# Optimization experiments

Measured on AMD Instinct MI355X. Metric: run time of the kernel, lower is better.

The kernel has to match this reference:

```python
import jax, jax.numpy as jnp
import numpy as np

N = 50000   # n_nodes
E = 500000  # n_edges
D = 128     # input_dim == hidden_dim
L = 2       # n_layers
K = 5       # Chebyshev filter size


def setup_inputs() -> dict:
    key = jax.random.key(0)
    k0, k1, k2, k3, k4 = jax.random.split(key, 5)
    scale = 1.0 / np.sqrt(D)
    return {
        "edge_index": jax.random.randint(k0, (2, E), 0, N),
        "edge_weight": jax.random.uniform(k1, (E,), dtype=jnp.float32),
        "emb": jax.random.uniform(k2, (N, D), dtype=jnp.float32, minval=-1.0, maxval=1.0),
        "Wx": jax.random.normal(k3, (L, 3, K, D, D), dtype=jnp.float32) * scale,
        "bx": jnp.zeros((L, 3, D), dtype=jnp.float32),
        "Wh": jax.random.normal(k4, (L, 3, K, D, D), dtype=jnp.float32) * scale,
        "bh": jnp.zeros((L, 3, D), dtype=jnp.float32),
    }


def reference(edge_index, edge_weight, emb, Wx, bx, Wh, bh):
    src, dst = edge_index[0], edge_index[1]
    # ChebConv sym-normalized scaled Laplacian with lambda_max=2:
    # L_hat = L - I = -D^{-1/2} A D^{-1/2} (zero diagonal)
    deg = jax.ops.segment_sum(edge_weight, src, num_segments=N)
    dinv = jnp.where(deg > 0, deg ** -0.5, 0.0)
    w = -dinv[src] * edge_weight * dinv[dst]  # [E]

    def prop(x):  # L_hat @ x via gather/scatter over edges
        return jax.ops.segment_sum(w[:, None] * x[src], dst, num_segments=N)

    def cheb(x, W, b):  # sum_k T_k(L_hat) x W_k + b
        Tx0 = x
        out = Tx0 @ W[0]
        Tx1 = prop(Tx0)
        out = out + Tx1 @ W[1]
        for k in range(2, K):
            Tx2 = 2.0 * prop(Tx1) - Tx0
            out = out + Tx2 @ W[k]
            Tx0, Tx1 = Tx1, Tx2
        return out + b

    x = emb
    hidden_states = []
    for l in range(L):
        H = jnp.ones((N, D), x.dtype)  # init__hidd: ones
        Z = jax.nn.sigmoid(cheb(x, Wx[l, 0], bx[l, 0]) + cheb(H, Wh[l, 0], bh[l, 0]))
        R = jax.nn.sigmoid(cheb(x, Wx[l, 1], bx[l, 1]) + cheb(H, Wh[l, 1], bh[l, 1]))
        Ht = jnp.tanh(cheb(x, Wx[l, 2], bx[l, 2]) + cheb(H * R, Wh[l, 2], bh[l, 2]))
        Hn = Z * H + (1.0 - Z) * Ht
        h = jax.nn.relu(Hn)  # dropout is identity in eval mode
        hidden_states.append(h)
        x = h
    return x  # == hidden_states[-1]
```

## Files before the change

### kernel.cpp

```cpp
#include <hip/hip_runtime.h>
#include <math.h>

#define NN 50000
#define EE 500000
#define DD 128
#define KK 5
#define LL 2

typedef _Float16 f16x8 __attribute__((ext_vector_type(8)));
typedef float f32x4 __attribute__((ext_vector_type(4)));

__device__ __forceinline__ ushort f2h(float x) {
    union { _Float16 h; ushort u; } v; v.h = (_Float16)x; return v.u;
}


__global__ __launch_bounds__(256) void edge_pass1(
    const int* __restrict__ src, const int* __restrict__ dst,
    const float* __restrict__ ew,
    float* __restrict__ deg, int* __restrict__ hist)
{
    int e = blockIdx.x * blockDim.x + threadIdx.x;
    if (e >= EE) return;
    atomicAdd(&deg[src[e]], ew[e]);
    atomicAdd(&hist[dst[e]], 1);
}

__global__ __launch_bounds__(256) void dinv_kernel(
    const float* __restrict__ deg, float* __restrict__ dinv)
{
    int i = blockIdx.x * blockDim.x + threadIdx.x;
    if (i >= NN) return;
    float d = deg[i];
    dinv[i] = (d > 0.f) ? (1.f / sqrtf(d)) : 0.f;
}

#define SCAN_C ((NN + 1023) / 1024)
__global__ __launch_bounds__(1024) void scan_kernel(
    const int* __restrict__ hist, int* __restrict__ row_ptr)
{
    __shared__ int sums[1024];
    const int t = threadIdx.x;
    const int base = t * SCAN_C;
    int local[SCAN_C];
    int s = 0;
#pragma unroll
    for (int j = 0; j < SCAN_C; ++j) {
        int i = base + j;
        int v = (i < NN) ? hist[i] : 0;
        s += v;
        local[j] = s;
    }
    sums[t] = s;
    __syncthreads();
    for (int off = 1; off < 1024; off <<= 1) {
        int v = (t >= off) ? sums[t - off] : 0;
        __syncthreads();
        sums[t] += v;
        __syncthreads();
    }
    int excl = sums[t] - s;
    if (t == 0) row_ptr[0] = 0;
#pragma unroll
    for (int j = 0; j < SCAN_C; ++j) {
        int i = base + j;
        if (i < NN) row_ptr[i + 1] = excl + local[j];
    }
}

__global__ __launch_bounds__(256) void copy_fill(
    const int* __restrict__ row_ptr, int* __restrict__ fill)
{
    int i = blockIdx.x * blockDim.x + threadIdx.x;
    if (i < NN) fill[i] = row_ptr[i];
}

__global__ __launch_bounds__(256) void edge_scatter(
    const int* __restrict__ src, const int* __restrict__ dst,
    const float* __restrict__ ew, const float* __restrict__ dinv,
    int* __restrict__ fill,
    int* __restrict__ src_srt, float* __restrict__ w_srt)
{
    int e = blockIdx.x * blockDim.x + threadIdx.x;
    if (e >= EE) return;
    int s = src[e], t = dst[e];
    float w = -dinv[s] * ew[e] * dinv[t];
    int pos = atomicAdd(&fill[t], 1);
    src_srt[pos] = s;
    w_srt[pos] = w;
}

__global__ __launch_bounds__(256) void propv_kernel(
    const int* __restrict__ rp, const int* __restrict__ ss, const float* __restrict__ sw,
    const float* __restrict__ tin, const float* __restrict__ tprev, float* __restrict__ tout,
    float alpha, float beta, int ones_in, int ones_prev)
{
    int i = blockIdx.x * blockDim.x + threadIdx.x;
    if (i >= NN) return;
    float acc = 0.f;
    int e0 = rp[i], e1 = rp[i + 1];
    int e = e0;
    for (; e + 4 <= e1; e += 4) {
        float t0 = ones_in ? 1.f : tin[ss[e]];
        float t1v = ones_in ? 1.f : tin[ss[e + 1]];
        float t2v = ones_in ? 1.f : tin[ss[e + 2]];
        float t3v = ones_in ? 1.f : tin[ss[e + 3]];
        acc += sw[e] * t0 + sw[e + 1] * t1v + sw[e + 2] * t2v + sw[e + 3] * t3v;
    }
    for (; e < e1; ++e) {
        float tv = ones_in ? 1.f : tin[ss[e]];
        acc += sw[e] * tv;
    }
    float pv = ones_prev ? 1.f : (tprev ? tprev[i] : 0.f);
    tout[i] = alpha * acc + beta * pv;
}

__global__ __launch_bounds__(128) void colsum_kernel(
    const float* __restrict__ Wh, float* __restrict__ scol)
{
    int b = blockIdx.x;
    int k = b % KK;
    int g = (b / KK) % 2;
    int l = b / (2 * KK);
    int d = threadIdx.x;
    const float* Wp = Wh + ((size_t)((l * 3 + g) * KK + k)) * DD * DD;
    float s = 0.f;
    for (int r = 0; r < DD; ++r) s += Wp[r * DD + d];
    scol[((size_t)((l * 2 + g) * KK + k)) * DD + d] = s;
}

__global__ __launch_bounds__(256) void wconv_f16(
    const float* __restrict__ W, ushort* __restrict__ out, int mode)
{
    int t = blockIdx.x;
    int st = (mode == 0) ? t : ((t / KK) * 3 + 2) * KK + (t % KK);
    const float* Wp = W + (size_t)st * DD * DD;
    ushort* op = out + (size_t)t * DD * DD;
    for (int idx = threadIdx.x; idx < DD * DD; idx += 256) {
        int rb = idx >> 7, c = idx & 127;
        float w = Wp[c * DD + rb];
        int byte = rb * 256 + (((c * 2) ^ ((rb & 7) << 4)));
        *(ushort*)((char*)op + byte) = f2h(w);
    }
}

__global__ __launch_bounds__(256) void f32_to_f16(
    const float* __restrict__ in, ushort* __restrict__ out, int n8)
{
    int i = blockIdx.x * blockDim.x + threadIdx.x;
    if (i >= n8) return;
    float4 a = ((const float4*)in)[i * 2];
    float4 b = ((const float4*)in)[i * 2 + 1];
    f16x8 o;
    o[0] = (_Float16)a.x; o[1] = (_Float16)a.y; o[2] = (_Float16)a.z; o[3] = (_Float16)a.w;
    o[4] = (_Float16)b.x; o[5] = (_Float16)b.y; o[6] = (_Float16)b.z; o[7] = (_Float16)b.w;
    ((f16x8*)out)[i] = o;
}

__global__ __launch_bounds__(256) void prop_mat(
    const int* __restrict__ rp, const int* __restrict__ ss, const float* __restrict__ sw,
    const ushort* __restrict__ x, const ushort* __restrict__ prev,
    ushort* __restrict__ out, float alpha, float beta)
{
    int node = blockIdx.x * 16 + (threadIdx.x >> 4);
    if (node >= NN) return;
    int lane = threadIdx.x & 15;
    int c = lane * 8;
    float acc[8];
#pragma unroll
    for (int j = 0; j < 8; ++j) acc[j] = 0.f;
    int e0 = rp[node], e1 = rp[node + 1];
    int e = e0;
    for (; e + 8 <= e1; e += 8) {
        int s0 = ss[e], s1 = ss[e + 1], s2 = ss[e + 2], s3 = ss[e + 3];
        int s4 = ss[e + 4], s5 = ss[e + 5], s6 = ss[e + 6], s7 = ss[e + 7];
        float w0 = sw[e], w1 = sw[e + 1], w2 = sw[e + 2], w3 = sw[e + 3];
        float w4 = sw[e + 4], w5 = sw[e + 5], w6 = sw[e + 6], w7 = sw[e + 7];
        f16x8 r0 = *(const f16x8*)(x + (size_t)s0 * DD + c);
        f16x8 r1 = *(const f16x8*)(x + (size_t)s1 * DD + c);
        f16x8 r2 = *(const f16x8*)(x + (size_t)s2 * DD + c);
        f16x8 r3 = *(const f16x8*)(x + (size_t)s3 * DD + c);
        f16x8 r4 = *(const f16x8*)(x + (size_t)s4 * DD + c);
        f16x8 r5 = *(const f16x8*)(x + (size_t)s5 * DD + c);
        f16x8 r6 = *(const f16x8*)(x + (size_t)s6 * DD + c);
        f16x8 r7 = *(const f16x8*)(x + (size_t)s7 * DD + c);
#pragma unroll
        for (int j = 0; j < 8; ++j)
            acc[j] += w0 * (float)r0[j] + w1 * (float)r1[j] + w2 * (float)r2[j] + w3 * (float)r3[j]
                    + w4 * (float)r4[j] + w5 * (float)r5[j] + w6 * (float)r6[j] + w7 * (float)r7[j];
    }
    for (; e + 4 <= e1; e += 4) {
        int s0 = ss[e], s1 = ss[e + 1], s2 = ss[e + 2], s3 = ss[e + 3];
        float w0 = sw[e], w1 = sw[e + 1], w2 = sw[e + 2], w3 = sw[e + 3];
        f16x8 r0 = *(const f16x8*)(x + (size_t)s0 * DD + c);
        f16x8 r1 = *(const f16x8*)(x + (size_t)s1 * DD + c);
        f16x8 r2 = *(const f16x8*)(x + (size_t)s2 * DD + c);
        f16x8 r3 = *(const f16x8*)(x + (size_t)s3 * DD + c);
#pragma unroll
        for (int j = 0; j < 8; ++j)
            acc[j] += w0 * (float)r0[j] + w1 * (float)r1[j] + w2 * (float)r2[j] + w3 * (float)r3[j];
    }
    for (; e < e1; ++e) {
        int s = ss[e];
        float w = sw[e];
        f16x8 r = *(const f16x8*)(x + (size_t)s * DD + c);
#pragma unroll
        for (int j = 0; j < 8; ++j) acc[j] += w * (float)r[j];
    }
    f16x8 o;
    if (beta != 0.f && prev) {
        f16x8 pv = *(const f16x8*)(prev + (size_t)node * DD + c);
#pragma unroll
        for (int j = 0; j < 8; ++j) o[j] = (_Float16)(alpha * acc[j] + beta * (float)pv[j]);
    } else {
#pragma unroll
        for (int j = 0; j < 8; ++j) o[j] = (_Float16)(alpha * acc[j]);
    }
    *(f16x8*)(out + (size_t)node * DD + c) = o;
}

__device__ __forceinline__ void mm_gate(
    const ushort* __restrict__ const* Ts, const ushort* __restrict__ Wg,
    ushort* Bs, int rowg0, int rowg1, bool ok0, bool ok1,
    int tid, int lk, f32x4 acc[2][8], int lr)
{
#pragma unroll
    for (int fr = 0; fr < 2; ++fr)
#pragma unroll
        for (int fc = 0; fc < 8; ++fc) acc[fr][fc] = (f32x4){0.f, 0.f, 0.f, 0.f};
#pragma unroll
    for (int k = 0; k < KK; ++k) {
        const ushort* Bg = Wg + (size_t)k * (DD * DD);
        __syncthreads();
#pragma unroll
        for (int i = 0; i < 8; ++i) {
            int off = i * 4096 + tid * 16;
            uint4 v = *(const uint4*)((const char*)Bg + off);
            *(uint4*)((char*)Bs + off) = v;
        }
        f16x8 a[2][4];
#pragma unroll
        for (int fr = 0; fr < 2; ++fr) {
            int rowg = fr ? rowg1 : rowg0;
            bool ok = fr ? ok1 : ok0;
            const ushort* rp2 = Ts[k] + (size_t)rowg * DD + lk * 8;
#pragma unroll
            for (int ko = 0; ko < 4; ++ko) {
                if (ok) a[fr][ko] = *(const f16x8*)(rp2 + ko * 32);
                else a[fr][ko] = (f16x8){0, 0, 0, 0, 0, 0, 0, 0};
            }
        }
        __syncthreads();
#pragma unroll
        for (int ko = 0; ko < 4; ++ko) {
            const int cb = ko * 64 + lk * 16;
#pragma unroll
            for (int fc = 0; fc < 8; ++fc) {
                int rb = fc * 16 + lr;
                int byte = (rb * 256 + cb) ^ ((rb & 7) << 4);
                f16x8 bfrag = *(const f16x8*)((const char*)Bs + byte);
                acc[0][fc] = __builtin_amdgcn_mfma_f32_16x16x32_f16(a[0][ko], bfrag, acc[0][fc], 0, 0, 0);
                acc[1][fc] = __builtin_amdgcn_mfma_f32_16x16x32_f16(a[1][ko], bfrag, acc[1][fc], 0, 0, 0);
            }
        }
    }
}

__device__ __forceinline__ int xcd_swz(int b, int nwg) {
    int xcd = b & 7, idx = b >> 3;
    int q = nwg >> 3, rr = nwg & 7;
    int start = (xcd < rr) ? xcd * (q + 1) : rr * (q + 1) + (xcd - rr) * q;
    return start + idx;
}

__global__ __launch_bounds__(256) void cheb_mm_mfma(
    const ushort* __restrict__ T0, const ushort* __restrict__ T1,
    const ushort* __restrict__ T2, const ushort* __restrict__ T3,
    const ushort* __restrict__ T4,
    const ushort* __restrict__ Wt, int gate_stride,
    float* __restrict__ outbase, size_t out_stride, int ngates)
{
    __shared__ ushort Bs[DD * DD];
    const int lin = xcd_swz(blockIdx.x, gridDim.x);
    const int tile = lin / ngates;
    const int g = lin - tile * ngates;

    const int tid = threadIdx.x;
    const int lane = tid & 63;
    const int wid = tid >> 6;
    const int lr = lane & 15;
    const int lk = lane >> 4;
    const int r0 = tile * 128;
    const ushort* Ts[5] = {T0, T1, T2, T3, T4};

    int rowg0 = r0 + wid * 32 + lr;
    int rowg1 = rowg0 + 16;
    bool ok0 = rowg0 < NN;
    bool ok1 = rowg1 < NN;

    f32x4 acc[2][8];
    mm_gate(Ts, Wt + (size_t)g * gate_stride, Bs, rowg0, rowg1, ok0, ok1, tid, lk, acc, lr);

    float* outp = outbase + (size_t)g * out_stride;
#pragma unroll
    for (int fr = 0; fr < 2; ++fr) {
#pragma unroll
        for (int j = 0; j < 4; ++j) {
            int grow = r0 + wid * 32 + fr * 16 + lk * 4 + j;
            if (grow < NN) {
#pragma unroll
                for (int fc = 0; fc < 8; ++fc) {
                    int col = fc * 16 + lr;
                    outp[(size_t)grow * DD + col] = acc[fr][fc][j];
                }
            }
        }
    }
}

__global__ __launch_bounds__(256) void cheb_mm_final(
    const ushort* __restrict__ T0, const ushort* __restrict__ T1,
    const ushort* __restrict__ T2, const ushort* __restrict__ T3,
    const ushort* __restrict__ T4,
    const ushort* __restrict__ Wt,
    const float* __restrict__ Xh, const float* __restrict__ Xz,
    const float* __restrict__ bx, const float* __restrict__ bh, int l,
    float* __restrict__ out, ushort* __restrict__ h16, int write_f32)
{
    __shared__ ushort Bs[DD * DD];
    const int tile = xcd_swz(blockIdx.x, gridDim.x);
    const int tid = threadIdx.x;
    const int lane = tid & 63;
    const int wid = tid >> 6;
    const int lr = lane & 15;
    const int lk = lane >> 4;
    const int r0 = tile * 128;
    const ushort* Ts[5] = {T0, T1, T2, T3, T4};

    int rowg0 = r0 + wid * 32 + lr;
    int rowg1 = rowg0 + 16;
    bool ok0 = rowg0 < NN;
    bool ok1 = rowg1 < NN;

    f32x4 acc[2][8];
    mm_gate(Ts, Wt, Bs, rowg0, rowg1, ok0, ok1, tid, lk, acc, lr);

    const float* b0 = bx + (size_t)(l * 3 + 2) * DD;
    const float* b1 = bh + (size_t)(l * 3 + 2) * DD;
#pragma unroll
    for (int fr = 0; fr < 2; ++fr) {
#pragma unroll
        for (int j = 0; j < 4; ++j) {
            int grow = r0 + wid * 32 + fr * 16 + lk * 4 + j;
            if (grow < NN) {
#pragma unroll
                for (int fc = 0; fc < 8; ++fc) {
                    int d = fc * 16 + lr;
                    size_t idx = (size_t)grow * DD + d;
                    float pre = acc[fr][fc][j] + Xh[idx] + b0[d] + b1[d];
                    float ht = tanhf(pre);
                    float z = Xz[idx];
                    float hn = z + (1.f - z) * ht;
                    float h = hn > 0.f ? hn : 0.f;
                    if (write_f32) out[idx] = h;
                    h16[idx] = f2h(h);
                }
            }
        }
    }
}

__global__ __launch_bounds__(256) void gate_zr_kernel(
    float* __restrict__ Xz, const float* __restrict__ Xr, ushort* __restrict__ Xr_f16,
    const float* __restrict__ tvec, const float* __restrict__ scol,
    const float* __restrict__ bx, const float* __restrict__ bh, int l)
{
    int idx = blockIdx.x * blockDim.x + threadIdx.x;
    if (idx >= NN * DD) return;
    int i = idx >> 7;
    int d = idx & 127;
    float t1 = tvec[i], t2 = tvec[NN + i], t3 = tvec[2 * NN + i], t4 = tvec[3 * NN + i];

    const float* s0 = scol + (size_t)((l * 2 + 0) * KK) * DD;
    float hz = s0[d] + t1 * s0[DD + d] + t2 * s0[2 * DD + d] + t3 * s0[3 * DD + d] + t4 * s0[4 * DD + d];
    float z = Xz[idx] + bx[(l * 3 + 0) * DD + d] + bh[(l * 3 + 0) * DD + d] + hz;
    Xz[idx] = 1.f / (1.f + expf(-z));

    const float* s1 = scol + (size_t)((l * 2 + 1) * KK) * DD;
    float hr = s1[d] + t1 * s1[DD + d] + t2 * s1[2 * DD + d] + t3 * s1[3 * DD + d] + t4 * s1[4 * DD + d];
    float r = Xr[idx] + bx[(l * 3 + 1) * DD + d] + bh[(l * 3 + 1) * DD + d] + hr;
    Xr_f16[idx] = f2h(1.f / (1.f + expf(-r)));
}


extern "C" void kernel_launch(void* const* d_in, const int* in_sizes, int n_in,
                              void* d_out, int out_size, void* d_ws, size_t ws_size,
                              hipStream_t stream)
{
    const int*   ei  = (const int*)d_in[0];
    const float* ew  = (const float*)d_in[1];
    const float* emb = (const float*)d_in[2];
    const float* Wx  = (const float*)d_in[3];
    const float* bx  = (const float*)d_in[4];
    const float* Wh  = (const float*)d_in[5];
    const float* bh  = (const float*)d_in[6];
    float* out = (float*)d_out;

    const int* src = ei;
    const int* dst = ei + EE;

    char* ws = (char*)d_ws;
    size_t off = 0;
    auto alloc = [&](size_t nbytes) -> char* {
        char* p = ws + off;
        off = (off + nbytes + 255) & ~(size_t)255;
        return p;
    };
    float*  deg     = (float*)alloc((size_t)NN * 4);
    float*  dinv    = (float*)alloc((size_t)NN * 4);
    int*    hist    = (int*)alloc((size_t)(NN + 1) * 4);
    int*    row_ptr = (int*)alloc((size_t)(NN + 1) * 4);
    int*    fill    = (int*)alloc((size_t)(NN + 1) * 4);
    int*    src_srt = (int*)alloc((size_t)EE * 4);
    float*  w_srt   = (float*)alloc((size_t)EE * 4);
    float*  tvec    = (float*)alloc((size_t)4 * NN * 4);
    float*  scol    = (float*)alloc((size_t)LL * 2 * KK * DD * 4);
    float*  X       = (float*)alloc((size_t)3 * NN * DD * 4);
    ushort* Th      = (ushort*)alloc((size_t)4 * NN * DD * 2);
    ushort* x_f16   = (ushort*)alloc((size_t)NN * DD * 2);
    ushort* Xr_f16  = (ushort*)alloc((size_t)NN * DD * 2);
    ushort* WxT     = (ushort*)alloc((size_t)LL * 3 * KK * DD * DD * 2);
    ushort* WhT2    = (ushort*)alloc((size_t)LL * KK * DD * DD * 2);
    (void)ws_size; (void)in_sizes; (void)n_in; (void)out_size;

    float* Xz = X;
    float* Xr = X + (size_t)NN * DD;
    float* Xh = X + (size_t)2 * NN * DD;
    ushort* T1 = Th;
    ushort* T2 = Th + (size_t)NN * DD;
    ushort* T3 = Th + (size_t)2 * NN * DD;
    ushort* T4 = Th + (size_t)3 * NN * DD;

    const int EG = (EE + 255) / 256;
    const int NG = (NN + 255) / 256;
    const int PG = (NN + 15) / 16;
    const int ELG = (NN * DD + 255) / 256;
    const int MMG = (NN + 127) / 128;
    const int CVG = (NN * DD / 8 + 255) / 256;
    const int GATE_STRIDE = KK * DD * DD;

    hipMemsetAsync(deg, 0, (size_t)NN * 4, stream);
    hipMemsetAsync(hist, 0, (size_t)(NN + 1) * 4, stream);

    edge_pass1<<<EG, 256, 0, stream>>>(src, dst, ew, deg, hist);
    dinv_kernel<<<NG, 256, 0, stream>>>(deg, dinv);
    scan_kernel<<<1, 1024, 0, stream>>>(hist, row_ptr);
    copy_fill<<<NG, 256, 0, stream>>>(row_ptr, fill);
    edge_scatter<<<EG, 256, 0, stream>>>(src, dst, ew, dinv, fill, src_srt, w_srt);

    float* t1 = tvec;
    float* t2 = tvec + NN;
    float* t3 = tvec + 2 * NN;
    float* t4 = tvec + 3 * NN;
    propv_kernel<<<NG, 256, 0, stream>>>(row_ptr, src_srt, w_srt, nullptr, nullptr, t1, 1.f,  0.f, 1, 0);
    propv_kernel<<<NG, 256, 0, stream>>>(row_ptr, src_srt, w_srt, t1, nullptr,      t2, 2.f, -1.f, 0, 1);
    propv_kernel<<<NG, 256, 0, stream>>>(row_ptr, src_srt, w_srt, t2, t1,           t3, 2.f, -1.f, 0, 0);
    propv_kernel<<<NG, 256, 0, stream>>>(row_ptr, src_srt, w_srt, t3, t2,           t4, 2.f, -1.f, 0, 0);

    colsum_kernel<<<LL * 2 * KK, 128, 0, stream>>>(Wh, scol);

    wconv_f16<<<LL * 3 * KK, 256, 0, stream>>>(Wx, WxT, 0);
    wconv_f16<<<LL * KK, 256, 0, stream>>>(Wh, WhT2, 1);

    f32_to_f16<<<CVG, 256, 0, stream>>>(emb, x_f16, NN * DD / 8);

    for (int l = 0; l < LL; ++l) {
        prop_mat<<<PG, 256, 0, stream>>>(row_ptr, src_srt, w_srt, x_f16, nullptr, T1, 1.f,  0.f);
        prop_mat<<<PG, 256, 0, stream>>>(row_ptr, src_srt, w_srt, T1,    x_f16,   T2, 2.f, -1.f);
        prop_mat<<<PG, 256, 0, stream>>>(row_ptr, src_srt, w_srt, T2,    T1,      T3, 2.f, -1.f);
        prop_mat<<<PG, 256, 0, stream>>>(row_ptr, src_srt, w_srt, T3,    T2,      T4, 2.f, -1.f);

        cheb_mm_mfma<<<MMG * 3, 256, 0, stream>>>(x_f16, T1, T2, T3, T4,
                                             WxT + (size_t)l * 3 * GATE_STRIDE, GATE_STRIDE,
                                             Xz, (size_t)NN * DD, 3);

        gate_zr_kernel<<<ELG, 256, 0, stream>>>(Xz, Xr, Xr_f16, tvec, scol, bx, bh, l);

        prop_mat<<<PG, 256, 0, stream>>>(row_ptr, src_srt, w_srt, Xr_f16, nullptr, T1, 1.f,  0.f);
        prop_mat<<<PG, 256, 0, stream>>>(row_ptr, src_srt, w_srt, T1,     Xr_f16,  T2, 2.f, -1.f);
        prop_mat<<<PG, 256, 0, stream>>>(row_ptr, src_srt, w_srt, T2,     T1,      T3, 2.f, -1.f);
        prop_mat<<<PG, 256, 0, stream>>>(row_ptr, src_srt, w_srt, T3,     T2,      T4, 2.f, -1.f);

        cheb_mm_final<<<MMG, 256, 0, stream>>>(Xr_f16, T1, T2, T3, T4,
                                               WhT2 + (size_t)l * GATE_STRIDE,
                                               Xh, Xz, bx, bh, l,
                                               out, x_f16, (l == LL - 1) ? 1 : 0);
    }
}
```

Before: 863.9 us.

## Store f16 node features in 16-column panels to localize SpMM gathers

The f16 feature matrices (x, T1..T4, Xr) now use a panel layout: 8 panels of 16 columns, each stored contiguously over all nodes. prop_mat gives each block one panel and 128 nodes, with two threads per node, so the gathered working set per panel is a 1.6 MB slice that can stay in cache instead of scattering across full 256-byte rows. The MFMA and gate kernels are adapted to read and write this layout. cheb_mm_final now uses 64-row tiles so more blocks are launched. Each gathered access is now only 32 bytes, and the edge index and weight lists are re-read once for each of the 8 panels.

After: 927.4 us. 1.07x slower.

```diff
diff --git a/kernel.cpp b/kernel.cpp
--- a/kernel.cpp
+++ b/kernel.cpp
@@ -6,6 +6,8 @@
 #define DD 128
 #define KK 5
 #define LL 2
+
+#define PSZ ((size_t)NN * 16)
 
 typedef _Float16 f16x8 __attribute__((ext_vector_type(8)));
 typedef float f32x4 __attribute__((ext_vector_type(4)));
@@ -144,17 +146,20 @@
     }
 }
 
-__global__ __launch_bounds__(256) void f32_to_f16(
+__global__ __launch_bounds__(256) void f32_to_f16_panel(
     const float* __restrict__ in, ushort* __restrict__ out, int n8)
 {
-    int i = blockIdx.x * blockDim.x + threadIdx.x;
-    if (i >= n8) return;
-    float4 a = ((const float4*)in)[i * 2];
-    float4 b = ((const float4*)in)[i * 2 + 1];
+    int j = blockIdx.x * blockDim.x + threadIdx.x;
+    if (j >= n8) return;
+    int flat = j * 8;
+    int i = flat >> 7;
+    int d0 = flat & 127;
+    float4 a = *(const float4*)(in + (size_t)i * DD + d0);
+    float4 b = *(const float4*)(in + (size_t)i * DD + d0 + 4);
     f16x8 o;
     o[0] = (_Float16)a.x; o[1] = (_Float16)a.y; o[2] = (_Float16)a.z; o[3] = (_Float16)a.w;
     o[4] = (_Float16)b.x; o[5] = (_Float16)b.y; o[6] = (_Float16)b.z; o[7] = (_Float16)b.w;
-    ((f16x8*)out)[i] = o;
+    *(f16x8*)(out + (size_t)(d0 >> 4) * PSZ + (size_t)i * 16 + (d0 & 15)) = o;
 }
 
 __global__ __launch_bounds__(256) void prop_mat(
@@ -162,10 +167,11 @@
     const ushort* __restrict__ x, const ushort* __restrict__ prev,
     ushort* __restrict__ out, float alpha, float beta)
 {
-    int node = blockIdx.x * 16 + (threadIdx.x >> 4);
+    const int p = blockIdx.x & 7;
+    const int node = (blockIdx.x >> 3) * 128 + (threadIdx.x >> 1);
     if (node >= NN) return;
-    int lane = threadIdx.x & 15;
-    int c = lane * 8;
+    const int half = (threadIdx.x & 1) * 8;
+    const ushort* xp = x + (size_t)p * PSZ + half;
     float acc[8];
 #pragma unroll
     for (int j = 0; j < 8; ++j) acc[j] = 0.f;
@@ -176,14 +182,14 @@
         int s4 = ss[e + 4], s5 = ss[e + 5], s6 = ss[e + 6], s7 = ss[e + 7];
         float w0 = sw[e], w1 = sw[e + 1], w2 = sw[e + 2], w3 = sw[e + 3];
         float w4 = sw[e + 4], w5 = sw[e + 5], w6 = sw[e + 6], w7 = sw[e + 7];
-        f16x8 r0 = *(const f16x8*)(x + (size_t)s0 * DD + c);
-        f16x8 r1 = *(const f16x8*)(x + (size_t)s1 * DD + c);
-        f16x8 r2 = *(const f16x8*)(x + (size_t)s2 * DD + c);
-        f16x8 r3 = *(const f16x8*)(x + (size_t)s3 * DD + c);
-        f16x8 r4 = *(const f16x8*)(x + (size_t)s4 * DD + c);
-        f16x8 r5 = *(const f16x8*)(x + (size_t)s5 * DD + c);
-        f16x8 r6 = *(const f16x8*)(x + (size_t)s6 * DD + c);
-        f16x8 r7 = *(const f16x8*)(x + (size_t)s7 * DD + c);
+        f16x8 r0 = *(const f16x8*)(xp + (size_t)s0 * 16);
+        f16x8 r1 = *(const f16x8*)(xp + (size_t)s1 * 16);
+        f16x8 r2 = *(const f16x8*)(xp + (size_t)s2 * 16);
+        f16x8 r3 = *(const f16x8*)(xp + (size_t)s3 * 16);
+        f16x8 r4 = *(const f16x8*)(xp + (size_t)s4 * 16);
+        f16x8 r5 = *(const f16x8*)(xp + (size_t)s5 * 16);
+        f16x8 r6 = *(const f16x8*)(xp + (size_t)s6 * 16);
+        f16x8 r7 = *(const f16x8*)(xp + (size_t)s7 * 16);
 #pragma unroll
         for (int j = 0; j < 8; ++j)
             acc[j] += w0 * (float)r0[j] + w1 * (float)r1[j] + w2 * (float)r2[j] + w3 * (float)r3[j]
@@ -192,10 +198,10 @@
     for (; e + 4 <= e1; e += 4) {
         int s0 = ss[e], s1 = ss[e + 1], s2 = ss[e + 2], s3 = ss[e + 3];
         float w0 = sw[e], w1 = sw[e + 1], w2 = sw[e + 2], w3 = sw[e + 3];
-        f16x8 r0 = *(const f16x8*)(x + (size_t)s0 * DD + c);
-        f16x8 r1 = *(const f16x8*)(x + (size_t)s1 * DD + c);
-        f16x8 r2 = *(const f16x8*)(x + (size_t)s2 * DD + c);
-        f16x8 r3 = *(const f16x8*)(x + (size_t)s3 * DD + c);
+        f16x8 r0 = *(const f16x8*)(xp + (size_t)s0 * 16);
+        f16x8 r1 = *(const f16x8*)(xp + (size_t)s1 * 16);
+        f16x8 r2 = *(const f16x8*)(xp + (size_t)s2 * 16);
+        f16x8 r3 = *(const f16x8*)(xp + (size_t)s3 * 16);
 #pragma unroll
         for (int j = 0; j < 8; ++j)
             acc[j] += w0 * (float)r0[j] + w1 * (float)r1[j] + w2 * (float)r2[j] + w3 * (float)r3[j];
@@ -203,29 +209,30 @@
     for (; e < e1; ++e) {
         int s = ss[e];
         float w = sw[e];
-        f16x8 r = *(const f16x8*)(x + (size_t)s * DD + c);
+        f16x8 r = *(const f16x8*)(xp + (size_t)s * 16);
 #pragma unroll
         for (int j = 0; j < 8; ++j) acc[j] += w * (float)r[j];
     }
     f16x8 o;
     if (beta != 0.f && prev) {
-        f16x8 pv = *(const f16x8*)(prev + (size_t)node * DD + c);
+        f16x8 pv = *(const f16x8*)(prev + (size_t)p * PSZ + (size_t)node * 16 + half);
 #pragma unroll
         for (int j = 0; j < 8; ++j) o[j] = (_Float16)(alpha * acc[j] + beta * (float)pv[j]);
     } else {
 #pragma unroll
         for (int j = 0; j < 8; ++j) o[j] = (_Float16)(alpha * acc[j]);
     }
-    *(f16x8*)(out + (size_t)node * DD + c) = o;
-}
-
+    *(f16x8*)(out + (size_t)p * PSZ + (size_t)node * 16 + half) = o;
+}
+
+template<int NFR>
 __device__ __forceinline__ void mm_gate(
     const ushort* __restrict__ const* Ts, const ushort* __restrict__ Wg,
-    ushort* Bs, int rowg0, int rowg1, bool ok0, bool ok1,
-    int tid, int lk, f32x4 acc[2][8], int lr)
-{
-#pragma unroll
-    for (int fr = 0; fr < 2; ++fr)
+    ushort* Bs, const int* rowg, const bool* ok,
+    int tid, int lk, f32x4 acc[NFR][8], int lr)
+{
+#pragma unroll
+    for (int fr = 0; fr < NFR; ++fr)
 #pragma unroll
         for (int fc = 0; fc < 8; ++fc) acc[fr][fc] = (f32x4){0.f, 0.f, 0.f, 0.f};
 #pragma unroll
@@ -238,15 +245,15 @@
             uint4 v = *(const uint4*)((const char*)Bg + off);
             *(uint4*)((char*)Bs + off) = v;
         }
-        f16x8 a[2][4];
-#pragma unroll
-        for (int fr = 0; fr < 2; ++fr) {
-            int rowg = fr ? rowg1 : rowg0;
-            bool ok = fr ? ok1 : ok0;
-            const ushort* rp2 = Ts[k] + (size_t)rowg * DD + lk * 8;
+        f16x8 a[NFR][4];
+#pragma unroll
+        for (int fr = 0; fr < NFR; ++fr) {
 #pragma unroll
             for (int ko = 0; ko < 4; ++ko) {
-                if (ok) a[fr][ko] = *(const f16x8*)(rp2 + ko * 32);
+                int col0 = lk * 8 + ko * 32;
+                const ushort* ap = Ts[k] + (size_t)(col0 >> 4) * PSZ
+                                 + (size_t)rowg[fr] * 16 + (col0 & 15);
+                if (ok[fr]) a[fr][ko] = *(const f16x8*)ap;
                 else a[fr][ko] = (f16x8){0, 0, 0, 0, 0, 0, 0, 0};
             }
         }
@@ -259,8 +266,9 @@
                 int rb = fc * 16 + lr;
                 int byte = (rb * 256 + cb) ^ ((rb & 7) << 4);
                 f16x8 bfrag = *(const f16x8*)((const char*)Bs + byte);
-                acc[0][fc] = __builtin_amdgcn_mfma_f32_16x16x32_f16(a[0][ko], bfrag, acc[0][fc], 0, 0, 0);
-                acc[1][fc] = __builtin_amdgcn_mfma_f32_16x16x32_f16(a[1][ko], bfrag, acc[1][fc], 0, 0, 0);
+#pragma unroll
+                for (int fr = 0; fr < NFR; ++fr)
+                    acc[fr][fc] = __builtin_amdgcn_mfma_f32_16x16x32_f16(a[fr][ko], bfrag, acc[fr][fc], 0, 0, 0);
             }
         }
     }
@@ -293,13 +301,11 @@
     const int r0 = tile * 128;
     const ushort* Ts[5] = {T0, T1, T2, T3, T4};
 
-    int rowg0 = r0 + wid * 32 + lr;
-    int rowg1 = rowg0 + 16;
-    bool ok0 = rowg0 < NN;
-    bool ok1 = rowg1 < NN;
+    int rowg[2] = {r0 + wid * 32 + lr, r0 + wid * 32 + lr + 16};
+    bool ok[2] = {rowg[0] < NN, rowg[1] < NN};
 
     f32x4 acc[2][8];
-    mm_gate(Ts, Wt + (size_t)g * gate_stride, Bs, rowg0, rowg1, ok0, ok1, tid, lk, acc, lr);
+    mm_gate<2>(Ts, Wt + (size_t)g * gate_stride, Bs, rowg, ok, tid, lk, acc, lr);
 
     float* outp = outbase + (size_t)g * out_stride;
 #pragma unroll
@@ -334,37 +340,32 @@
     const int wid = tid >> 6;
     const int lr = lane & 15;
     const int lk = lane >> 4;
-    const int r0 = tile * 128;
+    const int r0 = tile * 64;
     const ushort* Ts[5] = {T0, T1, T2, T3, T4};
 
-    int rowg0 = r0 + wid * 32 + lr;
-    int rowg1 = rowg0 + 16;
-    bool ok0 = rowg0 < NN;
-    bool ok1 = rowg1 < NN;
-
-    f32x4 acc[2][8];
-    mm_gate(Ts, Wt, Bs, rowg0, rowg1, ok0, ok1, tid, lk, acc, lr);
+    int rowg[1] = {r0 + wid * 16 + lr};
+    bool ok[1] = {rowg[0] < NN};
+
+    f32x4 acc[1][8];
+    mm_gate<1>(Ts, Wt, Bs, rowg, ok, tid, lk, acc, lr);
 
     const float* b0 = bx + (size_t)(l * 3 + 2) * DD;
     const float* b1 = bh + (size_t)(l * 3 + 2) * DD;
 #pragma unroll
-    for (int fr = 0; fr < 2; ++fr) {
-#pragma unroll
-        for (int j = 0; j < 4; ++j) {
-            int grow = r0 + wid * 32 + fr * 16 + lk * 4 + j;
-            if (grow < NN) {
-#pragma unroll
-                for (int fc = 0; fc < 8; ++fc) {
-                    int d = fc * 16 + lr;
-                    size_t idx = (size_t)grow * DD + d;
-                    float pre = acc[fr][fc][j] + Xh[idx] + b0[d] + b1[d];
-                    float ht = tanhf(pre);
-                    float z = Xz[idx];
-                    float hn = z + (1.f - z) * ht;
-                    float h = hn > 0.f ? hn : 0.f;
-                    if (write_f32) out[idx] = h;
-                    h16[idx] = f2h(h);
-                }
+    for (int j = 0; j < 4; ++j) {
+        int grow = r0 + wid * 16 + lk * 4 + j;
+        if (grow < NN) {
+#pragma unroll
+            for (int fc = 0; fc < 8; ++fc) {
+                int d = fc * 16 + lr;
+                size_t idx = (size_t)grow * DD + d;
+                float pre = acc[0][fc][j] + Xh[idx] + b0[d] + b1[d];
+                float ht = tanhf(pre);
+                float z = Xz[idx];
+                float hn = z + (1.f - z) * ht;
+                float h = hn > 0.f ? hn : 0.f;
+                if (write_f32) out[idx] = h;
+                else h16[(size_t)fc * PSZ + (size_t)grow * 16 + lr] = f2h(h);
             }
         }
     }
@@ -389,7 +390,7 @@
     const float* s1 = scol + (size_t)((l * 2 + 1) * KK) * DD;
     float hr = s1[d] + t1 * s1[DD + d] + t2 * s1[2 * DD + d] + t3 * s1[3 * DD + d] + t4 * s1[4 * DD + d];
     float r = Xr[idx] + bx[(l * 3 + 1) * DD + d] + bh[(l * 3 + 1) * DD + d] + hr;
-    Xr_f16[idx] = f2h(1.f / (1.f + expf(-r)));
+    Xr_f16[(size_t)(d >> 4) * PSZ + (size_t)i * 16 + (d & 15)] = f2h(1.f / (1.f + expf(-r)));
 }
 
 
@@ -443,9 +444,10 @@
 
     const int EG = (EE + 255) / 256;
     const int NG = (NN + 255) / 256;
-    const int PG = (NN + 15) / 16;
+    const int PG = ((NN + 127) / 128) * 8;
     const int ELG = (NN * DD + 255) / 256;
     const int MMG = (NN + 127) / 128;
+    const int MMG2 = (NN + 63) / 64;
     const int CVG = (NN * DD / 8 + 255) / 256;
     const int GATE_STRIDE = KK * DD * DD;
 
@@ -472,7 +474,7 @@
     wconv_f16<<<LL * 3 * KK, 256, 0, stream>>>(Wx, WxT, 0);
     wconv_f16<<<LL * KK, 256, 0, stream>>>(Wh, WhT2, 1);
 
-    f32_to_f16<<<CVG, 256, 0, stream>>>(emb, x_f16, NN * DD / 8);
+    f32_to_f16_panel<<<CVG, 256, 0, stream>>>(emb, x_f16, NN * DD / 8);
 
     for (int l = 0; l < LL; ++l) {
         prop_mat<<<PG, 256, 0, stream>>>(row_ptr, src_srt, w_srt, x_f16, nullptr, T1, 1.f,  0.f);
@@ -491,7 +493,7 @@
         prop_mat<<<PG, 256, 0, stream>>>(row_ptr, src_srt, w_srt, T2,     T1,      T3, 2.f, -1.f);
         prop_mat<<<PG, 256, 0, stream>>>(row_ptr, src_srt, w_srt, T3,     T2,      T4, 2.f, -1.f);
 
-        cheb_mm_final<<<MMG, 256, 0, stream>>>(Xr_f16, T1, T2, T3, T4,
+        cheb_mm_final<<<MMG2, 256, 0, stream>>>(Xr_f16, T1, T2, T3, T4,
                                                WhT2 + (size_t)l * GATE_STRIDE,
                                                Xh, Xz, bx, bh, l,
                                                out, x_f16, (l == LL - 1) ? 1 : 0);
```

## Degree-bucket prop rows, pre-fragment weights, drop LDS staging in cheb matmuls

Applied to the files above, without the earlier changes.

Nodes are sorted into degree buckets through a histogram, scan and scatter, and prop_mat walks them in that order so that the 16-lane groups in a block have similar edge counts. Weights are now stored in MFMA fragment order, which lets the matmul kernels read B fragments straight from global memory (through cache) with no LDS staging or __syncthreads. cheb_mm_final moves to 64-row tiles with one fragment row per wave, doubling its grid. The final layer no longer writes the unused f16 copy. The costs are scattered node order in prop_mat writes, repeated global loads of weights per wave, and three extra setup kernels.

Result: slower. 1.312 ms (+51.8%).

```diff
diff --git a/kernel.cpp b/kernel.cpp
--- a/kernel.cpp
+++ b/kernel.cpp
@@ -88,6 +88,44 @@
     int pos = atomicAdd(&fill[t], 1);
     src_srt[pos] = s;
     w_srt[pos] = w;
+}
+
+__global__ __launch_bounds__(256) void deg_bucket(
+    const int* __restrict__ row_ptr, int* __restrict__ bhist)
+{
+    int i = blockIdx.x * blockDim.x + threadIdx.x;
+    if (i >= NN) return;
+    int d = row_ptr[i + 1] - row_ptr[i];
+    if (d > 255) d = 255;
+    atomicAdd(&bhist[d], 1);
+}
+
+__global__ __launch_bounds__(256) void bucket_scan(
+    const int* __restrict__ bhist, int* __restrict__ bfill)
+{
+    __shared__ int buf[256];
+    int t = threadIdx.x;
+    int v0 = bhist[t];
+    buf[t] = v0;
+    __syncthreads();
+    for (int off = 1; off < 256; off <<= 1) {
+        int v = (t >= off) ? buf[t - off] : 0;
+        __syncthreads();
+        buf[t] += v;
+        __syncthreads();
+    }
+    bfill[t] = buf[t] - v0;
+}
+
+__global__ __launch_bounds__(256) void bucket_scatter(
+    const int* __restrict__ row_ptr, int* __restrict__ bfill, int* __restrict__ perm)
+{
+    int i = blockIdx.x * blockDim.x + threadIdx.x;
+    if (i >= NN) return;
+    int d = row_ptr[i + 1] - row_ptr[i];
+    if (d > 255) d = 255;
+    int pos = atomicAdd(&bfill[d], 1);
+    perm[pos] = i;
 }
 
 __global__ __launch_bounds__(256) void propv_kernel(
@@ -129,7 +167,7 @@
     scol[((size_t)((l * 2 + g) * KK + k)) * DD + d] = s;
 }
 
-__global__ __launch_bounds__(256) void wconv_f16(
+__global__ __launch_bounds__(256) void wconv_frag(
     const float* __restrict__ W, ushort* __restrict__ out, int mode)
 {
     int t = blockIdx.x;
@@ -137,10 +175,14 @@
     const float* Wp = W + (size_t)st * DD * DD;
     ushort* op = out + (size_t)t * DD * DD;
     for (int idx = threadIdx.x; idx < DD * DD; idx += 256) {
-        int rb = idx >> 7, c = idx & 127;
-        float w = Wp[c * DD + rb];
-        int byte = rb * 256 + (((c * 2) ^ ((rb & 7) << 4)));
-        *(ushort*)((char*)op + byte) = f2h(w);
+        int j  = idx & 7;
+        int lk = (idx >> 3) & 3;
+        int lr = (idx >> 5) & 15;
+        int fc = (idx >> 9) & 7;
+        int ko = idx >> 12;
+        int dout = fc * 16 + lr;
+        int din  = ko * 32 + lk * 8 + j;
+        op[idx] = f2h(Wp[din * DD + dout]);
     }
 }
 
@@ -159,11 +201,13 @@
 
 __global__ __launch_bounds__(256) void prop_mat(
     const int* __restrict__ rp, const int* __restrict__ ss, const float* __restrict__ sw,
+    const int* __restrict__ perm,
     const ushort* __restrict__ x, const ushort* __restrict__ prev,
     ushort* __restrict__ out, float alpha, float beta)
 {
-    int node = blockIdx.x * 16 + (threadIdx.x >> 4);
-    if (node >= NN) return;
+    int dense = blockIdx.x * 16 + (threadIdx.x >> 4);
+    if (dense >= NN) return;
+    int node = perm[dense];
     int lane = threadIdx.x & 15;
     int c = lane * 8;
     float acc[8];
@@ -219,48 +263,37 @@
     *(f16x8*)(out + (size_t)node * DD + c) = o;
 }
 
+template<int NFR>
 __device__ __forceinline__ void mm_gate(
     const ushort* __restrict__ const* Ts, const ushort* __restrict__ Wg,
-    ushort* Bs, int rowg0, int rowg1, bool ok0, bool ok1,
-    int tid, int lk, f32x4 acc[2][8], int lr)
-{
-#pragma unroll
-    for (int fr = 0; fr < 2; ++fr)
+    const int* rowg, const bool* ok, int lr, int lk, f32x4 acc[NFR][8])
+{
+#pragma unroll
+    for (int fr = 0; fr < NFR; ++fr)
 #pragma unroll
         for (int fc = 0; fc < 8; ++fc) acc[fr][fc] = (f32x4){0.f, 0.f, 0.f, 0.f};
 #pragma unroll
     for (int k = 0; k < KK; ++k) {
-        const ushort* Bg = Wg + (size_t)k * (DD * DD);
-        __syncthreads();
-#pragma unroll
-        for (int i = 0; i < 8; ++i) {
-            int off = i * 4096 + tid * 16;
-            uint4 v = *(const uint4*)((const char*)Bg + off);
-            *(uint4*)((char*)Bs + off) = v;
-        }
-        f16x8 a[2][4];
-#pragma unroll
-        for (int fr = 0; fr < 2; ++fr) {
-            int rowg = fr ? rowg1 : rowg0;
-            bool ok = fr ? ok1 : ok0;
-            const ushort* rp2 = Ts[k] + (size_t)rowg * DD + lk * 8;
+        f16x8 a[NFR][4];
+#pragma unroll
+        for (int fr = 0; fr < NFR; ++fr) {
+            const ushort* rp2 = Ts[k] + (size_t)rowg[fr] * DD + lk * 8;
 #pragma unroll
             for (int ko = 0; ko < 4; ++ko) {
-                if (ok) a[fr][ko] = *(const f16x8*)(rp2 + ko * 32);
+                if (ok[fr]) a[fr][ko] = *(const f16x8*)(rp2 + ko * 32);
                 else a[fr][ko] = (f16x8){0, 0, 0, 0, 0, 0, 0, 0};
             }
         }
-        __syncthreads();
+        const char* WB = (const char*)(Wg + (size_t)k * DD * DD);
+        const int lo = lr * 64 + lk * 16;
 #pragma unroll
         for (int ko = 0; ko < 4; ++ko) {
-            const int cb = ko * 64 + lk * 16;
 #pragma unroll
             for (int fc = 0; fc < 8; ++fc) {
-                int rb = fc * 16 + lr;
-                int byte = (rb * 256 + cb) ^ ((rb & 7) << 4);
-                f16x8 bfrag = *(const f16x8*)((const char*)Bs + byte);
-                acc[0][fc] = __builtin_amdgcn_mfma_f32_16x16x32_f16(a[0][ko], bfrag, acc[0][fc], 0, 0, 0);
-                acc[1][fc] = __builtin_amdgcn_mfma_f32_16x16x32_f16(a[1][ko], bfrag, acc[1][fc], 0, 0, 0);
+                f16x8 b = *(const f16x8*)(WB + ((ko * 8 + fc) << 10) + lo);
+#pragma unroll
+                for (int fr = 0; fr < NFR; ++fr)
+                    acc[fr][fc] = __builtin_amdgcn_mfma_f32_16x16x32_f16(a[fr][ko], b, acc[fr][fc], 0, 0, 0);
             }
         }
     }
@@ -280,7 +313,6 @@
     const ushort* __restrict__ Wt, int gate_stride,
     float* __restrict__ outbase, size_t out_stride, int ngates)
 {
-    __shared__ ushort Bs[DD * DD];
     const int lin = xcd_swz(blockIdx.x, gridDim.x);
     const int tile = lin / ngates;
     const int g = lin - tile * ngates;
@@ -293,13 +325,11 @@
     const int r0 = tile * 128;
     const ushort* Ts[5] = {T0, T1, T2, T3, T4};
 
-    int rowg0 = r0 + wid * 32 + lr;
-    int rowg1 = rowg0 + 16;
-    bool ok0 = rowg0 < NN;
-    bool ok1 = rowg1 < NN;
+    int rowg[2] = {r0 + wid * 32 + lr, r0 + wid * 32 + lr + 16};
+    bool ok[2] = {rowg[0] < NN, rowg[1] < NN};
 
     f32x4 acc[2][8];
-    mm_gate(Ts, Wt + (size_t)g * gate_stride, Bs, rowg0, rowg1, ok0, ok1, tid, lk, acc, lr);
+    mm_gate<2>(Ts, Wt + (size_t)g * gate_stride, rowg, ok, lr, lk, acc);
 
     float* outp = outbase + (size_t)g * out_stride;
 #pragma unroll
@@ -327,44 +357,38 @@
     const float* __restrict__ bx, const float* __restrict__ bh, int l,
     float* __restrict__ out, ushort* __restrict__ h16, int write_f32)
 {
-    __shared__ ushort Bs[DD * DD];
     const int tile = xcd_swz(blockIdx.x, gridDim.x);
     const int tid = threadIdx.x;
     const int lane = tid & 63;
     const int wid = tid >> 6;
     const int lr = lane & 15;
     const int lk = lane >> 4;
-    const int r0 = tile * 128;
+    const int r0 = tile * 64;
     const ushort* Ts[5] = {T0, T1, T2, T3, T4};
 
-    int rowg0 = r0 + wid * 32 + lr;
-    int rowg1 = rowg0 + 16;
-    bool ok0 = rowg0 < NN;
-    bool ok1 = rowg1 < NN;
-
-    f32x4 acc[2][8];
-    mm_gate(Ts, Wt, Bs, rowg0, rowg1, ok0, ok1, tid, lk, acc, lr);
+    int rowg[1] = {r0 + wid * 16 + lr};
+    bool ok[1] = {rowg[0] < NN};
+
+    f32x4 acc[1][8];
+    mm_gate<1>(Ts, Wt, rowg, ok, lr, lk, acc);
 
     const float* b0 = bx + (size_t)(l * 3 + 2) * DD;
     const float* b1 = bh + (size_t)(l * 3 + 2) * DD;
 #pragma unroll
-    for (int fr = 0; fr < 2; ++fr) {
-#pragma unroll
-        for (int j = 0; j < 4; ++j) {
-            int grow = r0 + wid * 32 + fr * 16 + lk * 4 + j;
-            if (grow < NN) {
-#pragma unroll
-                for (int fc = 0; fc < 8; ++fc) {
-                    int d = fc * 16 + lr;
-                    size_t idx = (size_t)grow * DD + d;
-                    float pre = acc[fr][fc][j] + Xh[idx] + b0[d] + b1[d];
-                    float ht = tanhf(pre);
-                    float z = Xz[idx];
-                    float hn = z + (1.f - z) * ht;
-                    float h = hn > 0.f ? hn : 0.f;
-                    if (write_f32) out[idx] = h;
-                    h16[idx] = f2h(h);
-                }
+    for (int j = 0; j < 4; ++j) {
+        int grow = r0 + wid * 16 + lk * 4 + j;
+        if (grow < NN) {
+#pragma unroll
+            for (int fc = 0; fc < 8; ++fc) {
+                int d = fc * 16 + lr;
+                size_t idx = (size_t)grow * DD + d;
+                float pre = acc[0][fc][j] + Xh[idx] + b0[d] + b1[d];
+                float ht = tanhf(pre);
+                float z = Xz[idx];
+                float hn = z + (1.f - z) * ht;
+                float h = hn > 0.f ? hn : 0.f;
+                if (write_f32) out[idx] = h;
+                else h16[idx] = f2h(h);
             }
         }
     }
@@ -423,6 +447,9 @@
     int*    fill    = (int*)alloc((size_t)(NN + 1) * 4);
     int*    src_srt = (int*)alloc((size_t)EE * 4);
     float*  w_srt   = (float*)alloc((size_t)EE * 4);
+    int*    bhist   = (int*)alloc(256 * 4);
+    int*    bfill   = (int*)alloc(256 * 4);
+    int*    perm    = (int*)alloc((size_t)NN * 4);
     float*  tvec    = (float*)alloc((size_t)4 * NN * 4);
     float*  scol    = (float*)alloc((size_t)LL * 2 * KK * DD * 4);
     float*  X       = (float*)alloc((size_t)3 * NN * DD * 4);
@@ -446,17 +473,23 @@
     const int PG = (NN + 15) / 16;
     const int ELG = (NN * DD + 255) / 256;
     const int MMG = (NN + 127) / 128;
+    const int MMG2 = (NN + 63) / 64;
     const int CVG = (NN * DD / 8 + 255) / 256;
     const int GATE_STRIDE = KK * DD * DD;
 
     hipMemsetAsync(deg, 0, (size_t)NN * 4, stream);
     hipMemsetAsync(hist, 0, (size_t)(NN + 1) * 4, stream);
+    hipMemsetAsync(bhist, 0, 256 * 4, stream);
 
     edge_pass1<<<EG, 256, 0, stream>>>(src, dst, ew, deg, hist);
     dinv_kernel<<<NG, 256, 0, stream>>>(deg, dinv);
     scan_kernel<<<1, 1024, 0, stream>>>(hist, row_ptr);
     copy_fill<<<NG, 256, 0, stream>>>(row_ptr, fill);
     edge_scatter<<<EG, 256, 0, stream>>>(src, dst, ew, dinv, fill, src_srt, w_srt);
+
+    deg_bucket<<<NG, 256, 0, stream>>>(row_ptr, bhist);
+    bucket_scan<<<1, 256, 0, stream>>>(bhist, bfill);
+    bucket_scatter<<<NG, 256, 0, stream>>>(row_ptr, bfill, perm);
 
     float* t1 = tvec;
     float* t2 = tvec + NN;
@@ -469,16 +502,16 @@
 
     colsum_kernel<<<LL * 2 * KK, 128, 0, stream>>>(Wh, scol);
 
-    wconv_f16<<<LL * 3 * KK, 256, 0, stream>>>(Wx, WxT, 0);
-    wconv_f16<<<LL * KK, 256, 0, stream>>>(Wh, WhT2, 1);
+    wconv_frag<<<LL * 3 * KK, 256, 0, stream>>>(Wx, WxT, 0);
+    wconv_frag<<<LL * KK, 256, 0, stream>>>(Wh, WhT2, 1);
 
     f32_to_f16<<<CVG, 256, 0, stream>>>(emb, x_f16, NN * DD / 8);
 
     for (int l = 0; l < LL; ++l) {
-        prop_mat<<<PG, 256, 0, stream>>>(row_ptr, src_srt, w_srt, x_f16, nullptr, T1, 1.f,  0.f);
-        prop_mat<<<PG, 256, 0, stream>>>(row_ptr, src_srt, w_srt, T1,    x_f16,   T2, 2.f, -1.f);
-        prop_mat<<<PG, 256, 0, stream>>>(row_ptr, src_srt, w_srt, T2,    T1,      T3, 2.f, -1.f);
-        prop_mat<<<PG, 256, 0, stream>>>(row_ptr, src_srt, w_srt, T3,    T2,      T4, 2.f, -1.f);
+        prop_mat<<<PG, 256, 0, stream>>>(row_ptr, src_srt, w_srt, perm, x_f16, nullptr, T1, 1.f,  0.f);
+        prop_mat<<<PG, 256, 0, stream>>>(row_ptr, src_srt, w_srt, perm, T1,    x_f16,   T2, 2.f, -1.f);
+        prop_mat<<<PG, 256, 0, stream>>>(row_ptr, src_srt, w_srt, perm, T2,    T1,      T3, 2.f, -1.f);
+        prop_mat<<<PG, 256, 0, stream>>>(row_ptr, src_srt, w_srt, perm, T3,    T2,      T4, 2.f, -1.f);
 
         cheb_mm_mfma<<<MMG * 3, 256, 0, stream>>>(x_f16, T1, T2, T3, T4,
                                              WxT + (size_t)l * 3 * GATE_STRIDE, GATE_STRIDE,
@@ -486,12 +519,12 @@
 
         gate_zr_kernel<<<ELG, 256, 0, stream>>>(Xz, Xr, Xr_f16, tvec, scol, bx, bh, l);
 
-        prop_mat<<<PG, 256, 0, stream>>>(row_ptr, src_srt, w_srt, Xr_f16, nullptr, T1, 1.f,  0.f);
-        prop_mat<<<PG, 256, 0, stream>>>(row_ptr, src_srt, w_srt, T1,     Xr_f16,  T2, 2.f, -1.f);
-        prop_mat<<<PG, 256, 0, stream>>>(row_ptr, src_srt, w_srt, T2,     T1,      T3, 2.f, -1.f);
-        prop_mat<<<PG, 256, 0, stream>>>(row_ptr, src_srt, w_srt, T3,     T2,      T4, 2.f, -1.f);
-
-        cheb_mm_final<<<MMG, 256, 0, stream>>>(Xr_f16, T1, T2, T3, T4,
+        prop_mat<<<PG, 256, 0, stream>>>(row_ptr, src_srt, w_srt, perm, Xr_f16, nullptr, T1, 1.f,  0.f);
+        prop_mat<<<PG, 256, 0, stream>>>(row_ptr, src_srt, w_srt, perm, T1,     Xr_f16,  T2, 2.f, -1.f);
+        prop_mat<<<PG, 256, 0, stream>>>(row_ptr, src_srt, w_srt, perm, T2,     T1,      T3, 2.f, -1.f);
+        prop_mat<<<PG, 256, 0, stream>>>(row_ptr, src_srt, w_srt, perm, T3,     T2,      T4, 2.f, -1.f);
+
+        cheb_mm_final<<<MMG2, 256, 0, stream>>>(Xr_f16, T1, T2, T3, T4,
                                                WhT2 + (size_t)l * GATE_STRIDE,
                                                Xh, Xz, bx, bh, l,
                                                out, x_f16, (l == LL - 1) ? 1 : 0);
```
